# Optimization experiments

Hardware: AMD Instinct MI355X
Metric: run time of the kernel (lower is better)

## Reference

```python
import jax, jax.numpy as jnp
import numpy as np

B, S, D, H = 8, 1024, 1024, 16
HD = D // H  # head dim 64
NUM_REL = 7


def setup_inputs() -> dict:
    key = jax.random.key(0)
    ks = jax.random.split(key, 10)
    s = 0.02
    return {
        "hidden_states": jax.random.normal(ks[0], (B, S, D), dtype=jnp.float32),
        "attention_mask": jnp.zeros((B, 1, 1, S), dtype=jnp.float32),
        "relation": jax.random.randint(ks[1], (B, S, S), 0, NUM_REL, dtype=jnp.int32),
        "Wq": jax.random.normal(ks[2], (D, D), dtype=jnp.float32) * s,
        "bq": jnp.zeros((D,), dtype=jnp.float32),
        "Wk": jax.random.normal(ks[3], (D, D), dtype=jnp.float32) * s,
        "bk": jnp.zeros((D,), dtype=jnp.float32),
        "Wv": jax.random.normal(ks[4], (D, D), dtype=jnp.float32) * s,
        "bv": jnp.zeros((D,), dtype=jnp.float32),
        "rel_emb": jax.random.normal(ks[5], (NUM_REL, H), dtype=jnp.float32) * s,
    }


def reference(hidden_states, attention_mask, relation, Wq, bq, Wk, bk, Wv, bv, rel_emb):
    def heads(x):  # [B,S,D] -> [B,H,S,HD]
        return x.reshape(B, S, H, HD).transpose(0, 2, 1, 3)

    q = heads(hidden_states @ Wq.T + bq)
    k = heads(hidden_states @ Wk.T + bk)
    v = heads(hidden_states @ Wv.T + bv)

    scores = jnp.einsum("bhqd,bhkd->bhqk", q, k) / jnp.sqrt(jnp.float32(HD))
    # relation bias: gather [B,S,S,H] then move H to dim 1
    rel_bias = rel_emb[relation].transpose(0, 3, 1, 2)  # [B,H,S,S]
    scores = scores + rel_bias + attention_mask
    probs = jax.nn.softmax(scores, axis=-1)  # dropout is identity in eval
    ctx = jnp.einsum("bhqk,bhkd->bhqd", probs, v)
    return ctx.transpose(0, 2, 1, 3).reshape(B, S, D)
```

## Files before the change

### kernel.cpp

```cpp
#include <hip/hip_runtime.h>

#define NB 8
#define NS 1024
#define ND 1024
#define NH 16
#define NHD 64

typedef __attribute__((ext_vector_type(8))) short bf16x8;
typedef __attribute__((ext_vector_type(4))) float f32x4;
typedef __attribute__((ext_vector_type(4))) unsigned int u32x4;

#define GLOAD_LDS16(g, l) __builtin_amdgcn_global_load_lds(                    \
    (const __attribute__((address_space(1))) void*)(g),                        \
    (__attribute__((address_space(3))) void*)(l), 16, 0, 0)

static __device__ __forceinline__ unsigned short f2bf(float f) {
    unsigned int u = __builtin_bit_cast(unsigned int, f);
    unsigned int r = u + 0x7fffu + ((u >> 16) & 1u);
    return (unsigned short)(r >> 16);
}

static __device__ __forceinline__ unsigned int cvtpk(float lo, float hi) {
    unsigned int r;
    asm("v_cvt_pk_bf16_f32 %0, %1, %2" : "=v"(r) : "v"(lo), "v"(hi));
    return r;
}

static __device__ __forceinline__ float ldre(const float* t, unsigned int byteoff) {
    return *reinterpret_cast<const float*>(reinterpret_cast<const char*>(t) + byteoff);
}

__global__ void cvt_f32_bf16(const float* __restrict__ in, unsigned short* __restrict__ out, int n) {
    int i = (blockIdx.x * blockDim.x + threadIdx.x) * 4;
    if (i >= n) return;
    float4 v = *reinterpret_cast<const float4*>(in + i);
    ushort4 o;
    o.x = f2bf(v.x); o.y = f2bf(v.y); o.z = f2bf(v.z); o.w = f2bf(v.w);
    *reinterpret_cast<ushort4*>(out + i) = o;
}

__global__ void cvt_w3(const float* __restrict__ Wq, const float* __restrict__ Wk,
                       const float* __restrict__ Wv, unsigned short* __restrict__ out) {
    const float* src = (blockIdx.y == 0) ? Wq : (blockIdx.y == 1) ? Wk : Wv;
    int i = (blockIdx.x * blockDim.x + threadIdx.x) * 4;
    float4 v = *reinterpret_cast<const float4*>(src + i);
    ushort4 o;
    o.x = f2bf(v.x); o.y = f2bf(v.y); o.z = f2bf(v.z); o.w = f2bf(v.w);
    *reinterpret_cast<ushort4*>(out + (size_t)blockIdx.y * (ND * ND) + i) = o;
}

__global__ void pack_rel8(const int* __restrict__ rel, unsigned int* __restrict__ out) {
    int i = blockIdx.x * blockDim.x + threadIdx.x;
    int4 v = reinterpret_cast<const int4*>(rel)[i];
    out[i] = ((unsigned)v.x << 2) | ((unsigned)v.y << 10) |
             ((unsigned)v.z << 18) | ((unsigned)v.w << 26);
}

__global__ __launch_bounds__(256) void qkv_gemm(
    const unsigned short* __restrict__ A,
    const unsigned short* __restrict__ Wq, const unsigned short* __restrict__ Wk,
    const unsigned short* __restrict__ Wv,
    const float* __restrict__ bq, const float* __restrict__ bk, const float* __restrict__ bv,
    const float* __restrict__ mask,
    unsigned short* __restrict__ Qo, unsigned short* __restrict__ Ko, unsigned short* __restrict__ Vo)
{
    const int z = blockIdx.z;
    const unsigned short* W = (z == 0) ? Wq : (z == 1) ? Wk : Wv;
    const float* bias = (z == 0) ? bq : (z == 1) ? bk : bv;
    const int m0 = blockIdx.x * 128;
    const int n0 = blockIdx.y * 128;
    const float LOG2E = 1.4426950408889634f;
    const float QSCL = 0.125f * 1.4426950408889634f;

    __shared__ unsigned short S[2][128][64];

    const int tid = threadIdx.x;
    const int lane = tid & 63;
    const int wave = tid >> 6;
    const int wm = wave >> 1, wn = wave & 1;
    const int g = lane >> 4, l15 = lane & 15;

    f32x4 acc[4][4] = {};

    const int crow = lane >> 3;
    const int gcol = ((lane & 7) ^ crow) * 8;
    const int kofs = g * 8;

    for (int kb = 0; kb < ND; kb += 64) {
#pragma unroll
        for (int cc = 0; cc < 4; ++cc) {
            int ch = wave * 4 + cc;
            GLOAD_LDS16(&A[(size_t)(m0 + ch * 8 + crow) * ND + kb + gcol], &S[0][ch * 8][0]);
            GLOAD_LDS16(&W[(size_t)(n0 + ch * 8 + crow) * ND + kb + gcol], &S[1][ch * 8][0]);
        }
        __syncthreads();
#pragma unroll
        for (int kk = 0; kk < 2; ++kk) {
            const int colx = (kk * 32 + kofs) ^ ((lane & 7) * 8);
            bf16x8 af[4], bfr[4];
#pragma unroll
            for (int i = 0; i < 4; ++i) {
                af[i]  = *reinterpret_cast<const bf16x8*>(&S[0][wm * 64 + i * 16 + l15][colx]);
                bfr[i] = *reinterpret_cast<const bf16x8*>(&S[1][wn * 64 + i * 16 + l15][colx]);
            }
#pragma unroll
            for (int mi = 0; mi < 4; ++mi)
#pragma unroll
                for (int ni = 0; ni < 4; ++ni)
                    acc[mi][ni] = __builtin_amdgcn_mfma_f32_16x16x32_bf16(af[mi], bfr[ni], acc[mi][ni], 0, 0, 0);
        }
        __syncthreads();
    }

    __syncthreads();
    char* L = reinterpret_cast<char*>(&S[0][0][0]) + wave * 8192;
    const int rrow = lane >> 3, cb = lane & 7;

    if (z == 2) {
#pragma unroll
        for (int ni = 0; ni < 4; ++ni) {
            int n = n0 + wn * 64 + ni * 16 + l15;
            int nl = ni * 16 + l15;
            float bv_ = bias[n];
#pragma unroll
            for (int mi = 0; mi < 4; ++mi) {
                int m = m0 + wm * 64 + mi * 16 + g * 4;
                int b = m >> 10, s = m & 1023;
                float4 mv = *reinterpret_cast<const float4*>(&mask[(size_t)b * NS + s]);
                unsigned int lo = cvtpk((acc[mi][ni][0] + bv_) * exp2f(mv.x * LOG2E),
                                        (acc[mi][ni][1] + bv_) * exp2f(mv.y * LOG2E));
                unsigned int hi = cvtpk((acc[mi][ni][2] + bv_) * exp2f(mv.z * LOG2E),
                                        (acc[mi][ni][3] + bv_) * exp2f(mv.w * LOG2E));
                int ml = mi * 16 + g * 4;
                int off = nl * 128 + (((ml >> 3) ^ (nl & 7)) * 16) + (ml & 7) * 2;
                *reinterpret_cast<uint2*>(L + off) = make_uint2(lo, hi);
            }
        }
#pragma unroll
        for (int p = 0; p < 8; ++p) {
            int nl = p * 8 + rrow;
            u32x4 v = *reinterpret_cast<const u32x4*>(L + nl * 128 + ((cb ^ (nl & 7)) * 16));
            int n = n0 + wn * 64 + nl;
            int h = n >> 6, hd = n & 63;
            int m = m0 + wm * 64 + cb * 8;
            int b = m >> 10, s = m & 1023;
            *reinterpret_cast<u32x4*>(&Vo[(((size_t)b * NH + h) * NHD + hd) * NS + s]) = v;
        }
    } else {
        unsigned short* O = (z == 0) ? Qo : Ko;
#pragma unroll
        for (int ni = 0; ni < 4; ++ni) {
            int n = n0 + wn * 64 + ni * 16 + l15;
            int nl = ni * 16 + l15;
            float bv_ = bias[n];
            int c16 = nl >> 3, bin = (nl & 7) * 2;
#pragma unroll
            for (int mi = 0; mi < 4; ++mi) {
#pragma unroll
                for (int r = 0; r < 4; ++r) {
                    int ml = mi * 16 + g * 4 + r;
                    float v = acc[mi][ni][r] + bv_;
                    if (z == 0) v *= QSCL;
                    int off = ml * 128 + ((c16 ^ (ml & 7)) * 16) + bin;
                    *reinterpret_cast<unsigned short*>(L + off) = f2bf(v);
                }
            }
        }
#pragma unroll
        for (int p = 0; p < 8; ++p) {
            int ml = p * 8 + rrow;
            u32x4 v = *reinterpret_cast<const u32x4*>(L + ml * 128 + ((cb ^ (ml & 7)) * 16));
            int m = m0 + wm * 64 + ml;
            int b = m >> 10, s = m & 1023;
            int n = n0 + wn * 64 + cb * 8;
            int h = n >> 6, hd = n & 63;
            *reinterpret_cast<u32x4*>(&O[(((size_t)b * NH + h) * NS + s) * NHD + hd]) = v;
        }
    }
}

__global__ __launch_bounds__(512) void flash_attn(
    const unsigned short* __restrict__ Q, const unsigned short* __restrict__ Kb,
    const unsigned short* __restrict__ Vt,
    const unsigned char* __restrict__ rel8, const float* __restrict__ rel_emb,
    const float* __restrict__ mask, float* __restrict__ out)
{
    const int id = blockIdx.x;
    const int b = id & 7;
    const int h = (id >> 3) & 15;
    const int q0 = (id >> 7) * 128;
    const int tid = threadIdx.x, lane = tid & 63, wave = tid >> 6;
    const int g = lane >> 4, l15 = lane & 15;

    __shared__ unsigned short Ks[2][64][64];
    __shared__ unsigned short Vs[2][64][64];
    __shared__ unsigned short s_emask[NS];
    __shared__ float s_re2[8];
    const float LOG2E = 1.4426950408889634f;
    if (tid < 7) s_re2[tid] = rel_emb[tid * NH + h] * LOG2E - 4.0f;

    const unsigned short* Qh = Q  + (((size_t)b * NH + h) * NS) * NHD;
    const unsigned short* Kh = Kb + (((size_t)b * NH + h) * NS) * NHD;
    const unsigned short* Vh = Vt + (((size_t)b * NH + h) * NHD) * NS;
    const int qg = q0 + wave * 16 + l15;
    const unsigned char* __restrict__ relrow = rel8 + (size_t)b * NS * NS + (size_t)qg * NS;
    const float* __restrict__ maskb = mask + (size_t)b * NS;

    bf16x8 qa[2];
    qa[0] = *reinterpret_cast<const bf16x8*>(&Qh[(size_t)qg * NHD + g * 8]);
    qa[1] = *reinterpret_cast<const bf16x8*>(&Qh[(size_t)qg * NHD + 32 + g * 8]);

    f32x4 ctx[4] = {};
    f32x4 l_acc = {};
    float mofs = 0.f;
    bool everscaled = false;

    const int crow = lane >> 3;
    const int gcol = ((lane & 7) ^ crow) * 8;
    const int swz8 = (lane & 7) * 8;

    const int rho = wave * 8 + crow;
    const int kvperm = ((rho >> 5) << 5) + (((rho >> 2) & 3) << 3)
                     + (((rho >> 4) & 1) << 2) + (rho & 3);

#define STAGE(buf, kv)                                                                          \
    {                                                                                           \
        GLOAD_LDS16(&Kh[(size_t)((kv) + kvperm) * NHD + gcol], &Ks[buf][wave * 8][0]);          \
        GLOAD_LDS16(&Vh[(size_t)(wave * 8 + crow) * NS + (kv) + gcol], &Vs[buf][wave * 8][0]);  \
    }

#define LOADRM(S, t0)                                                                \
    {                                                                                \
        r##S##a = *reinterpret_cast<const uint2*>(&relrow[(t0) * 64 + 8 * g]);       \
        r##S##b = *reinterpret_cast<const uint2*>(&relrow[(t0) * 64 + 32 + 8 * g]);  \
    }

    uint2 rAa, rAb, rBa, rBb;

    STAGE(0, 0)
    LOADRM(A, 0)
    s_emask[tid] = f2bf(exp2f(maskb[tid] * LOG2E));
    s_emask[tid + 512] = f2bf(exp2f(maskb[tid + 512] * LOG2E));
    __syncthreads();

#define BODY(cur, S, SN, tc, tn)                                               \
  {                                                                            \
    if ((tn) < 16) {                                                           \
      STAGE(cur ^ 1, (tn) * 64)                                                \
      LOADRM(SN, tn)                                                           \
    }                                                                          \
    f32x4 sc[4] = {};                                                          \
    __builtin_amdgcn_s_setprio(1);                                             \
    _Pragma("unroll")                                                          \
    for (int kk = 0; kk < 2; ++kk) {                                           \
      const int colx = (kk * 32 + g * 8) ^ swz8;                               \
      _Pragma("unroll")                                                        \
      for (int tt = 0; tt < 4; ++tt) {                                         \
        bf16x8 kfrag = *reinterpret_cast<const bf16x8*>(&Ks[cur][tt * 16 + l15][colx]); \
        sc[tt] = __builtin_amdgcn_mfma_f32_16x16x32_bf16(kfrag, qa[kk], sc[tt], 0, 0, 0); \
      }                                                                        \
    }                                                                          \
    __builtin_amdgcn_s_setprio(0);                                             \
    const unsigned int rw[4] = {r##S##a.x, r##S##a.y, r##S##b.x, r##S##b.y};   \
    float pmax = -1e30f;                                                       \
    _Pragma("unroll")                                                          \
    for (int tt = 0; tt < 4; ++tt) {                                           \
      float v0 = sc[tt][0] + ldre(s_re2, rw[tt] & 0xFF);                       \
      float v1 = sc[tt][1] + ldre(s_re2, (rw[tt] >> 8) & 0xFF);                \
      float v2 = sc[tt][2] + ldre(s_re2, (rw[tt] >> 16) & 0xFF);               \
      float v3 = sc[tt][3] + ldre(s_re2, rw[tt] >> 24);                        \
      sc[tt][0] = v0; sc[tt][1] = v1; sc[tt][2] = v2; sc[tt][3] = v3;          \
      pmax = fmaxf(pmax, fmaxf(fmaxf(v0, v1), fmaxf(v2, v3)));                 \
    }                                                                          \
    if (!__all(pmax <= mofs + 8.0f)) {                                         \
      float pm = fmaxf(pmax, __shfl_xor(pmax, 16));                            \
      pm = fmaxf(pm, __shfl_xor(pm, 32));                                      \
      float mnew = fmaxf(mofs, pm);                                            \
      float alpha = exp2f(mofs - mnew);                                        \
      mofs = mnew;                                                             \
      everscaled = true;                                                       \
      float ar[4];                                                             \
      _Pragma("unroll")                                                        \
      for (int r = 0; r < 4; ++r) ar[r] = __shfl(alpha, 4 * g + r);            \
      _Pragma("unroll")                                                        \
      for (int r = 0; r < 4; ++r) l_acc[r] *= ar[r];                           \
      _Pragma("unroll")                                                        \
      for (int ht = 0; ht < 4; ++ht)                                           \
        _Pragma("unroll")                                                      \
        for (int r = 0; r < 4; ++r) ctx[ht][r] *= ar[r];                       \
    }                                                                          \
    unsigned int pw[8];                                                        \
    if (!everscaled) {                                                         \
      _Pragma("unroll")                                                        \
      for (int tt = 0; tt < 4; ++tt) {                                         \
        pw[2 * tt]     = cvtpk(exp2f(sc[tt][0]), exp2f(sc[tt][1]));            \
        pw[2 * tt + 1] = cvtpk(exp2f(sc[tt][2]), exp2f(sc[tt][3]));            \
      }                                                                        \
    } else {                                                                   \
      _Pragma("unroll")                                                        \
      for (int tt = 0; tt < 4; ++tt) {                                         \
        pw[2 * tt]     = cvtpk(exp2f(sc[tt][0] - mofs), exp2f(sc[tt][1] - mofs)); \
        pw[2 * tt + 1] = cvtpk(exp2f(sc[tt][2] - mofs), exp2f(sc[tt][3] - mofs)); \
      }                                                                        \
    }                                                                          \
    __builtin_amdgcn_s_setprio(1);                                             \
    _Pragma("unroll")                                                          \
    for (int kk = 0; kk < 2; ++kk) {                                           \
      u32x4 paw = {pw[4 * kk], pw[4 * kk + 1], pw[4 * kk + 2], pw[4 * kk + 3]};\
      bf16x8 pa = __builtin_bit_cast(bf16x8, paw);                             \
      const int colx = (kk * 32 + g * 8) ^ swz8;                               \
      bf16x8 mfr = *reinterpret_cast<const bf16x8*>(&s_emask[(tc) * 64 + kk * 32 + g * 8]); \
      l_acc = __builtin_amdgcn_mfma_f32_16x16x32_bf16(pa, mfr, l_acc, 0, 0, 0); \
      _Pragma("unroll")                                                        \
      for (int ht = 0; ht < 4; ++ht) {                                         \
        bf16x8 bfrag = *reinterpret_cast<const bf16x8*>(&Vs[cur][ht * 16 + l15][colx]); \
        ctx[ht] = __builtin_amdgcn_mfma_f32_16x16x32_bf16(pa, bfrag, ctx[ht], 0, 0, 0); \
      }                                                                        \
    }                                                                          \
    __builtin_amdgcn_s_setprio(0);                                             \
    __syncthreads();                                                           \
  }

    for (int t = 0; t < 16; t += 2) {
        BODY(0, A, B, t, t + 1)
        BODY(1, B, A, t + 1, t + 2)
    }
#undef BODY
#undef LOADRM
#undef STAGE

    float linv[4];
#pragma unroll
    for (int r = 0; r < 4; ++r) linv[r] = 1.0f / l_acc[r];
#pragma unroll
    for (int ht = 0; ht < 4; ++ht) {
        int hd = ht * 16 + l15;
#pragma unroll
        for (int r = 0; r < 4; ++r) {
            int qo = q0 + wave * 16 + 4 * g + r;
            out[((size_t)b * NS + qo) * ND + h * NHD + hd] = ctx[ht][r] * linv[r];
        }
    }
}

extern "C" void kernel_launch(void* const* d_in, const int* in_sizes, int n_in,
                              void* d_out, int out_size, void* d_ws, size_t ws_size,
                              hipStream_t stream) {
    const float* hs      = (const float*)d_in[0];
    const float* mask    = (const float*)d_in[1];
    const int*   rel     = (const int*)d_in[2];
    const float* Wq      = (const float*)d_in[3];
    const float* bq      = (const float*)d_in[4];
    const float* Wk      = (const float*)d_in[5];
    const float* bk      = (const float*)d_in[6];
    const float* Wv      = (const float*)d_in[7];
    const float* bv      = (const float*)d_in[8];
    const float* rel_emb = (const float*)d_in[9];
    float* out = (float*)d_out;

    char* ws = (char*)d_ws;
    unsigned short* q_bf  = (unsigned short*)(ws);
    unsigned short* k_bf  = (unsigned short*)(ws + ((size_t)16 << 20));
    unsigned short* vt_bf = (unsigned short*)(ws + ((size_t)32 << 20));
    unsigned short* hs_bf = (unsigned short*)(ws + ((size_t)48 << 20));
    unsigned short* w_bf  = (unsigned short*)(ws + ((size_t)64 << 20));
    unsigned char*  rel8  = (unsigned char*)(ws + ((size_t)48 << 20));

    const int nhs = NB * NS * ND;
    const int nw  = ND * ND;
    cvt_f32_bf16<<<nhs / 4 / 256, 256, 0, stream>>>(hs, hs_bf, nhs);
    cvt_w3<<<dim3(nw / 4 / 256, 3), 256, 0, stream>>>(Wq, Wk, Wv, w_bf);

    qkv_gemm<<<dim3((NB * NS) / 128, ND / 128, 3), 256, 0, stream>>>(
        hs_bf, w_bf, w_bf + (size_t)nw, w_bf + (size_t)2 * nw,
        bq, bk, bv, mask, q_bf, k_bf, vt_bf);

    pack_rel8<<<(NB * NS * NS / 4) / 256, 256, 0, stream>>>(rel, (unsigned int*)rel8);

    flash_attn<<<1024, 512, 0, stream>>>(
        q_bf, k_bf, vt_bf, rel8, rel_emb, mask, out);
}
```

Before: 156.7 us.

## Process two 16-row query tiles per wave in flash attention with 256 threads

Each wave now handles 32 query rows as two 16-row tiles, so K and V fragments read from LDS are reused across two MFMA chains, and the block shrinks to 4 waves for the same 128-query tile. This halves LDS fragment reads per query row and gives more independent MFMA work per wave. In exchange, register pressure roughly doubles for accumulators, and there are fewer waves per block to hide latency. The rescale branch now fires whenever either tile needs it.

```diff
diff --git a/kernel.cpp b/kernel.cpp
--- a/kernel.cpp
+++ b/kernel.cpp
@@ -179,7 +179,7 @@
     }
 }
 
-__global__ __launch_bounds__(512) void flash_attn(
+__global__ __launch_bounds__(256) void flash_attn(
     const unsigned short* __restrict__ Q, const unsigned short* __restrict__ Kb,
     const unsigned short* __restrict__ Vt,
     const unsigned char* __restrict__ rel8, const float* __restrict__ rel_emb,
@@ -202,45 +202,57 @@
     const unsigned short* Qh = Q  + (((size_t)b * NH + h) * NS) * NHD;
     const unsigned short* Kh = Kb + (((size_t)b * NH + h) * NS) * NHD;
     const unsigned short* Vh = Vt + (((size_t)b * NH + h) * NHD) * NS;
-    const int qg = q0 + wave * 16 + l15;
-    const unsigned char* __restrict__ relrow = rel8 + (size_t)b * NS * NS + (size_t)qg * NS;
+    const int qg0 = q0 + wave * 32 + l15;
+    const int qg1 = qg0 + 16;
+    const unsigned char* __restrict__ relrow0 = rel8 + (size_t)b * NS * NS + (size_t)qg0 * NS;
+    const unsigned char* __restrict__ relrow1 = relrow0 + 16 * NS;
     const float* __restrict__ maskb = mask + (size_t)b * NS;
 
-    bf16x8 qa[2];
-    qa[0] = *reinterpret_cast<const bf16x8*>(&Qh[(size_t)qg * NHD + g * 8]);
-    qa[1] = *reinterpret_cast<const bf16x8*>(&Qh[(size_t)qg * NHD + 32 + g * 8]);
-
-    f32x4 ctx[4] = {};
-    f32x4 l_acc = {};
-    float mofs = 0.f;
+    bf16x8 qa0[2], qa1[2];
+    qa0[0] = *reinterpret_cast<const bf16x8*>(&Qh[(size_t)qg0 * NHD + g * 8]);
+    qa0[1] = *reinterpret_cast<const bf16x8*>(&Qh[(size_t)qg0 * NHD + 32 + g * 8]);
+    qa1[0] = *reinterpret_cast<const bf16x8*>(&Qh[(size_t)qg1 * NHD + g * 8]);
+    qa1[1] = *reinterpret_cast<const bf16x8*>(&Qh[(size_t)qg1 * NHD + 32 + g * 8]);
+
+    f32x4 ctx0[4] = {}, ctx1[4] = {};
+    f32x4 l_acc0 = {}, l_acc1 = {};
+    float mofs0 = 0.f, mofs1 = 0.f;
     bool everscaled = false;
 
     const int crow = lane >> 3;
     const int gcol = ((lane & 7) ^ crow) * 8;
     const int swz8 = (lane & 7) * 8;
 
-    const int rho = wave * 8 + crow;
-    const int kvperm = ((rho >> 5) << 5) + (((rho >> 2) & 3) << 3)
-                     + (((rho >> 4) & 1) << 2) + (rho & 3);
-
-#define STAGE(buf, kv)                                                                          \
-    {                                                                                           \
-        GLOAD_LDS16(&Kh[(size_t)((kv) + kvperm) * NHD + gcol], &Ks[buf][wave * 8][0]);          \
-        GLOAD_LDS16(&Vh[(size_t)(wave * 8 + crow) * NS + (kv) + gcol], &Vs[buf][wave * 8][0]);  \
-    }
-
-#define LOADRM(S, t0)                                                                \
-    {                                                                                \
-        r##S##a = *reinterpret_cast<const uint2*>(&relrow[(t0) * 64 + 8 * g]);       \
-        r##S##b = *reinterpret_cast<const uint2*>(&relrow[(t0) * 64 + 32 + 8 * g]);  \
-    }
-
-    uint2 rAa, rAb, rBa, rBb;
+    const int rho0 = wave * 16 + crow;
+    const int rho1 = rho0 + 8;
+#define KVPERM(r) ((((r) >> 5) << 5) + ((((r) >> 2) & 3) << 3) + ((((r) >> 4) & 1) << 2) + ((r) & 3))
+    const int kvp0 = KVPERM(rho0);
+    const int kvp1 = KVPERM(rho1);
+#undef KVPERM
+
+#define STAGE(buf, kv)                                                                              \
+    {                                                                                               \
+        GLOAD_LDS16(&Kh[(size_t)((kv) + kvp0) * NHD + gcol], &Ks[buf][wave * 16][0]);               \
+        GLOAD_LDS16(&Kh[(size_t)((kv) + kvp1) * NHD + gcol], &Ks[buf][wave * 16 + 8][0]);           \
+        GLOAD_LDS16(&Vh[(size_t)(wave * 16 + crow) * NS + (kv) + gcol], &Vs[buf][wave * 16][0]);    \
+        GLOAD_LDS16(&Vh[(size_t)(wave * 16 + 8 + crow) * NS + (kv) + gcol], &Vs[buf][wave * 16 + 8][0]); \
+    }
+
+#define LOADRM(S, t0)                                                                  \
+    {                                                                                  \
+        r##S##a0 = *reinterpret_cast<const uint2*>(&relrow0[(t0) * 64 + 8 * g]);       \
+        r##S##b0 = *reinterpret_cast<const uint2*>(&relrow0[(t0) * 64 + 32 + 8 * g]);  \
+        r##S##a1 = *reinterpret_cast<const uint2*>(&relrow1[(t0) * 64 + 8 * g]);       \
+        r##S##b1 = *reinterpret_cast<const uint2*>(&relrow1[(t0) * 64 + 32 + 8 * g]);  \
+    }
+
+    uint2 rAa0, rAb0, rAa1, rAb1, rBa0, rBb0, rBa1, rBb1;
 
     STAGE(0, 0)
     LOADRM(A, 0)
-    s_emask[tid] = f2bf(exp2f(maskb[tid] * LOG2E));
-    s_emask[tid + 512] = f2bf(exp2f(maskb[tid + 512] * LOG2E));
+#pragma unroll
+    for (int i = 0; i < 4; ++i)
+        s_emask[tid + i * 256] = f2bf(exp2f(maskb[tid + i * 256] * LOG2E));
     __syncthreads();
 
 #define BODY(cur, S, SN, tc, tn)                                               \
@@ -249,73 +261,99 @@
       STAGE(cur ^ 1, (tn) * 64)                                                \
       LOADRM(SN, tn)                                                           \
     }                                                                          \
-    f32x4 sc[4] = {};                                                          \
+    f32x4 sc0[4] = {}, sc1[4] = {};                                            \
     __builtin_amdgcn_s_setprio(1);                                             \
     _Pragma("unroll")                                                          \
     for (int kk = 0; kk < 2; ++kk) {                                           \
       const int colx = (kk * 32 + g * 8) ^ swz8;                               \
-      _Pragma("unroll")                                                        \
-      for (int tt = 0; tt < 4; ++tt) {                                         \
-        bf16x8 kfrag = *reinterpret_cast<const bf16x8*>(&Ks[cur][tt * 16 + l15][colx]); \
-        sc[tt] = __builtin_amdgcn_mfma_f32_16x16x32_bf16(kfrag, qa[kk], sc[tt], 0, 0, 0); \
-      }                                                                        \
+      bf16x8 kfrag[4];                                                         \
+      _Pragma("unroll")                                                        \
+      for (int tt = 0; tt < 4; ++tt)                                           \
+        kfrag[tt] = *reinterpret_cast<const bf16x8*>(&Ks[cur][tt * 16 + l15][colx]); \
+      _Pragma("unroll")                                                        \
+      for (int tt = 0; tt < 4; ++tt)                                           \
+        sc0[tt] = __builtin_amdgcn_mfma_f32_16x16x32_bf16(kfrag[tt], qa0[kk], sc0[tt], 0, 0, 0); \
+      _Pragma("unroll")                                                        \
+      for (int tt = 0; tt < 4; ++tt)                                           \
+        sc1[tt] = __builtin_amdgcn_mfma_f32_16x16x32_bf16(kfrag[tt], qa1[kk], sc1[tt], 0, 0, 0); \
     }                                                                          \
     __builtin_amdgcn_s_setprio(0);                                             \
-    const unsigned int rw[4] = {r##S##a.x, r##S##a.y, r##S##b.x, r##S##b.y};   \
-    float pmax = -1e30f;                                                       \
+    const unsigned int rw0[4] = {r##S##a0.x, r##S##a0.y, r##S##b0.x, r##S##b0.y}; \
+    const unsigned int rw1[4] = {r##S##a1.x, r##S##a1.y, r##S##b1.x, r##S##b1.y}; \
+    float pmax0 = -1e30f, pmax1 = -1e30f;                                      \
     _Pragma("unroll")                                                          \
     for (int tt = 0; tt < 4; ++tt) {                                           \
-      float v0 = sc[tt][0] + ldre(s_re2, rw[tt] & 0xFF);                       \
-      float v1 = sc[tt][1] + ldre(s_re2, (rw[tt] >> 8) & 0xFF);                \
-      float v2 = sc[tt][2] + ldre(s_re2, (rw[tt] >> 16) & 0xFF);               \
-      float v3 = sc[tt][3] + ldre(s_re2, rw[tt] >> 24);                        \
-      sc[tt][0] = v0; sc[tt][1] = v1; sc[tt][2] = v2; sc[tt][3] = v3;          \
-      pmax = fmaxf(pmax, fmaxf(fmaxf(v0, v1), fmaxf(v2, v3)));                 \
-    }                                                                          \
-    if (!__all(pmax <= mofs + 8.0f)) {                                         \
-      float pm = fmaxf(pmax, __shfl_xor(pmax, 16));                            \
-      pm = fmaxf(pm, __shfl_xor(pm, 32));                                      \
-      float mnew = fmaxf(mofs, pm);                                            \
-      float alpha = exp2f(mofs - mnew);                                        \
-      mofs = mnew;                                                             \
+      float a0 = sc0[tt][0] + ldre(s_re2, rw0[tt] & 0xFF);                     \
+      float a1 = sc0[tt][1] + ldre(s_re2, (rw0[tt] >> 8) & 0xFF);              \
+      float a2 = sc0[tt][2] + ldre(s_re2, (rw0[tt] >> 16) & 0xFF);             \
+      float a3 = sc0[tt][3] + ldre(s_re2, rw0[tt] >> 24);                      \
+      sc0[tt][0] = a0; sc0[tt][1] = a1; sc0[tt][2] = a2; sc0[tt][3] = a3;      \
+      pmax0 = fmaxf(pmax0, fmaxf(fmaxf(a0, a1), fmaxf(a2, a3)));               \
+      float b0 = sc1[tt][0] + ldre(s_re2, rw1[tt] & 0xFF);                     \
+      float b1 = sc1[tt][1] + ldre(s_re2, (rw1[tt] >> 8) & 0xFF);              \
+      float b2 = sc1[tt][2] + ldre(s_re2, (rw1[tt] >> 16) & 0xFF);             \
+      float b3 = sc1[tt][3] + ldre(s_re2, rw1[tt] >> 24);                      \
+      sc1[tt][0] = b0; sc1[tt][1] = b1; sc1[tt][2] = b2; sc1[tt][3] = b3;      \
+      pmax1 = fmaxf(pmax1, fmaxf(fmaxf(b0, b1), fmaxf(b2, b3)));               \
+    }                                                                          \
+    if (!__all((pmax0 <= mofs0 + 8.0f) && (pmax1 <= mofs1 + 8.0f))) {          \
+      float pm0 = fmaxf(pmax0, __shfl_xor(pmax0, 16));                         \
+      pm0 = fmaxf(pm0, __shfl_xor(pm0, 32));                                   \
+      float pm1 = fmaxf(pmax1, __shfl_xor(pmax1, 16));                         \
+      pm1 = fmaxf(pm1, __shfl_xor(pm1, 32));                                   \
+      float mn0 = fmaxf(mofs0, pm0), mn1 = fmaxf(mofs1, pm1);                  \
+      float al0 = exp2f(mofs0 - mn0), al1 = exp2f(mofs1 - mn1);                \
+      mofs0 = mn0; mofs1 = mn1;                                                \
       everscaled = true;                                                       \
-      float ar[4];                                                             \
-      _Pragma("unroll")                                                        \
-      for (int r = 0; r < 4; ++r) ar[r] = __shfl(alpha, 4 * g + r);            \
-      _Pragma("unroll")                                                        \
-      for (int r = 0; r < 4; ++r) l_acc[r] *= ar[r];                           \
+      float ar0[4], ar1[4];                                                    \
+      _Pragma("unroll")                                                        \
+      for (int r = 0; r < 4; ++r) { ar0[r] = __shfl(al0, 4 * g + r); ar1[r] = __shfl(al1, 4 * g + r); } \
+      _Pragma("unroll")                                                        \
+      for (int r = 0; r < 4; ++r) { l_acc0[r] *= ar0[r]; l_acc1[r] *= ar1[r]; }\
       _Pragma("unroll")                                                        \
       for (int ht = 0; ht < 4; ++ht)                                           \
         _Pragma("unroll")                                                      \
-        for (int r = 0; r < 4; ++r) ctx[ht][r] *= ar[r];                       \
-    }                                                                          \
-    unsigned int pw[8];                                                        \
+        for (int r = 0; r < 4; ++r) { ctx0[ht][r] *= ar0[r]; ctx1[ht][r] *= ar1[r]; } \
+    }                                                                          \
+    unsigned int pw0[8], pw1[8];                                               \
     if (!everscaled) {                                                         \
       _Pragma("unroll")                                                        \
       for (int tt = 0; tt < 4; ++tt) {                                         \
-        pw[2 * tt]     = cvtpk(exp2f(sc[tt][0]), exp2f(sc[tt][1]));            \
-        pw[2 * tt + 1] = cvtpk(exp2f(sc[tt][2]), exp2f(sc[tt][3]));            \
+        pw0[2 * tt]     = cvtpk(exp2f(sc0[tt][0]), exp2f(sc0[tt][1]));         \
+        pw0[2 * tt + 1] = cvtpk(exp2f(sc0[tt][2]), exp2f(sc0[tt][3]));         \
+        pw1[2 * tt]     = cvtpk(exp2f(sc1[tt][0]), exp2f(sc1[tt][1]));         \
+        pw1[2 * tt + 1] = cvtpk(exp2f(sc1[tt][2]), exp2f(sc1[tt][3]));         \
       }                                                                        \
     } else {                                                                   \
       _Pragma("unroll")                                                        \
       for (int tt = 0; tt < 4; ++tt) {                                         \
-        pw[2 * tt]     = cvtpk(exp2f(sc[tt][0] - mofs), exp2f(sc[tt][1] - mofs)); \
-        pw[2 * tt + 1] = cvtpk(exp2f(sc[tt][2] - mofs), exp2f(sc[tt][3] - mofs)); \
+        pw0[2 * tt]     = cvtpk(exp2f(sc0[tt][0] - mofs0), exp2f(sc0[tt][1] - mofs0)); \
+        pw0[2 * tt + 1] = cvtpk(exp2f(sc0[tt][2] - mofs0), exp2f(sc0[tt][3] - mofs0)); \
+        pw1[2 * tt]     = cvtpk(exp2f(sc1[tt][0] - mofs1), exp2f(sc1[tt][1] - mofs1)); \
+        pw1[2 * tt + 1] = cvtpk(exp2f(sc1[tt][2] - mofs1), exp2f(sc1[tt][3] - mofs1)); \
       }                                                                        \
     }                                                                          \
     __builtin_amdgcn_s_setprio(1);                                             \
     _Pragma("unroll")                                                          \
     for (int kk = 0; kk < 2; ++kk) {                                           \
-      u32x4 paw = {pw[4 * kk], pw[4 * kk + 1], pw[4 * kk + 2], pw[4 * kk + 3]};\
-      bf16x8 pa = __builtin_bit_cast(bf16x8, paw);                             \
       const int colx = (kk * 32 + g * 8) ^ swz8;                               \
+      bf16x8 bfrag[4];                                                         \
+      _Pragma("unroll")                                                        \
+      for (int ht = 0; ht < 4; ++ht)                                           \
+        bfrag[ht] = *reinterpret_cast<const bf16x8*>(&Vs[cur][ht * 16 + l15][colx]); \
       bf16x8 mfr = *reinterpret_cast<const bf16x8*>(&s_emask[(tc) * 64 + kk * 32 + g * 8]); \
-      l_acc = __builtin_amdgcn_mfma_f32_16x16x32_bf16(pa, mfr, l_acc, 0, 0, 0); \
-      _Pragma("unroll")                                                        \
-      for (int ht = 0; ht < 4; ++ht) {                                         \
-        bf16x8 bfrag = *reinterpret_cast<const bf16x8*>(&Vs[cur][ht * 16 + l15][colx]); \
-        ctx[ht] = __builtin_amdgcn_mfma_f32_16x16x32_bf16(pa, bfrag, ctx[ht], 0, 0, 0); \
-      }                                                                        \
+      u32x4 paw0 = {pw0[4 * kk], pw0[4 * kk + 1], pw0[4 * kk + 2], pw0[4 * kk + 3]}; \
+      bf16x8 pa0 = __builtin_bit_cast(bf16x8, paw0);                           \
+      l_acc0 = __builtin_amdgcn_mfma_f32_16x16x32_bf16(pa0, mfr, l_acc0, 0, 0, 0); \
+      _Pragma("unroll")                                                        \
+      for (int ht = 0; ht < 4; ++ht)                                           \
+        ctx0[ht] = __builtin_amdgcn_mfma_f32_16x16x32_bf16(pa0, bfrag[ht], ctx0[ht], 0, 0, 0); \
+      u32x4 paw1 = {pw1[4 * kk], pw1[4 * kk + 1], pw1[4 * kk + 2], pw1[4 * kk + 3]}; \
+      bf16x8 pa1 = __builtin_bit_cast(bf16x8, paw1);                           \
+      l_acc1 = __builtin_amdgcn_mfma_f32_16x16x32_bf16(pa1, mfr, l_acc1, 0, 0, 0); \
+      _Pragma("unroll")                                                        \
+      for (int ht = 0; ht < 4; ++ht)                                           \
+        ctx1[ht] = __builtin_amdgcn_mfma_f32_16x16x32_bf16(pa1, bfrag[ht], ctx1[ht], 0, 0, 0); \
     }                                                                          \
     __builtin_amdgcn_s_setprio(0);                                             \
     __syncthreads();                                                           \
@@ -329,16 +367,17 @@
 #undef LOADRM
 #undef STAGE
 
-    float linv[4];
-#pragma unroll
-    for (int r = 0; r < 4; ++r) linv[r] = 1.0f / l_acc[r];
+    float li0[4], li1[4];
+#pragma unroll
+    for (int r = 0; r < 4; ++r) { li0[r] = 1.0f / l_acc0[r]; li1[r] = 1.0f / l_acc1[r]; }
 #pragma unroll
     for (int ht = 0; ht < 4; ++ht) {
         int hd = ht * 16 + l15;
 #pragma unroll
         for (int r = 0; r < 4; ++r) {
-            int qo = q0 + wave * 16 + 4 * g + r;
-            out[((size_t)b * NS + qo) * ND + h * NHD + hd] = ctx[ht][r] * linv[r];
+            int qo0 = q0 + wave * 32 + 4 * g + r;
+            out[((size_t)b * NS + qo0) * ND + h * NHD + hd] = ctx0[ht][r] * li0[r];
+            out[((size_t)b * NS + qo0 + 16) * ND + h * NHD + hd] = ctx1[ht][r] * li1[r];
         }
     }
 }
@@ -377,6 +416,6 @@
 
     pack_rel8<<<(NB * NS * NS / 4) / 256, 256, 0, stream>>>(rel, (unsigned int*)rel8);
 
-    flash_attn<<<1024, 512, 0, stream>>>(
+    flash_attn<<<1024, 256, 0, stream>>>(
         q_bf, k_bf, vt_bf, rel8, rel_emb, mask, out);
 }
```

Result: slower. 167.2 us (+6.7%).
